# Kernel tuning notes

Measured on AMD Instinct MI355X. Metric: run time of the kernel, lower is better.

## Reference

```python
import jax, jax.numpy as jnp
import numpy as np

D_MODEL = 1024
NHEAD = 16
D_HEAD = D_MODEL // NHEAD


def setup_inputs() -> dict:
    key = jax.random.key(0)
    ks = jax.random.split(key, 9)
    B, S = 2, 2048
    scale = 1.0 / np.sqrt(D_MODEL)
    x = jax.random.normal(ks[0], (B, S, D_MODEL), dtype=jnp.float32)
    Wq = jax.random.normal(ks[1], (D_MODEL, D_MODEL), dtype=jnp.float32) * scale
    Wk = jax.random.normal(ks[2], (D_MODEL, D_MODEL), dtype=jnp.float32) * scale
    Wv = jax.random.normal(ks[3], (D_MODEL, D_MODEL), dtype=jnp.float32) * scale
    Wo = jax.random.normal(ks[4], (D_MODEL, D_MODEL), dtype=jnp.float32) * scale
    bq = jax.random.normal(ks[5], (D_MODEL,), dtype=jnp.float32) * 0.01
    bk = jax.random.normal(ks[6], (D_MODEL,), dtype=jnp.float32) * 0.01
    bv = jax.random.normal(ks[7], (D_MODEL,), dtype=jnp.float32) * 0.01
    bo = jax.random.normal(ks[8], (D_MODEL,), dtype=jnp.float32) * 0.01
    return {"x": x, "Wq": Wq, "bq": bq, "Wk": Wk, "bk": bk,
            "Wv": Wv, "bv": bv, "Wo": Wo, "bo": bo}


def reference(x, Wq, bq, Wk, bk, Wv, bv, Wo, bo):
    B, S, D = x.shape
    H, Dh = NHEAD, D_HEAD
    # projections; weights stored as (in, out) so y = x @ W + b
    def split_heads(t):  # [B,S,D] -> [B,H,S,Dh]
        return t.reshape(B, S, H, Dh).transpose(0, 2, 1, 3)
    q = split_heads(x @ Wq + bq)
    k = split_heads(x @ Wk + bk)
    v = split_heads(x @ Wv + bv)
    scale = 1.0 / jnp.sqrt(jnp.asarray(Dh, dtype=x.dtype))
    attn = jnp.einsum("bhqd,bhkd->bhqk", q, k) * scale  # [B,H,S,S]
    attn = jax.nn.softmax(attn, axis=-1)
    out = jnp.einsum("bhqk,bhkd->bhqd", attn, v)  # [B,H,S,Dh]
    out = out.transpose(0, 2, 1, 3).reshape(B, S, D)
    return out @ Wo + bo
```

## Files before the change

### kernel.cpp

```cpp
#include <hip/hip_runtime.h>
#include <hip/hip_bf16.h>
#include <stdint.h>
#include <stddef.h>

typedef __bf16 b16;
typedef __bf16 b16x4 __attribute__((ext_vector_type(4)));
typedef __bf16 b16x8 __attribute__((ext_vector_type(8)));
typedef short  s16x4 __attribute__((ext_vector_type(4)));
typedef float  f32x4 __attribute__((ext_vector_type(4)));

#define LOG2E 1.4426950408889634f
#define QSCALE (0.125f * LOG2E)

#if __has_builtin(__builtin_amdgcn_exp2f)
#define EXP2F(x) __builtin_amdgcn_exp2f(x)
#else
#define EXP2F(x) exp2f(x)
#endif

typedef __attribute__((address_space(1))) void gvoid;
typedef __attribute__((address_space(3))) void svoid;

__device__ __forceinline__ void async_cp16(void* lds, const void* g) {
    __builtin_amdgcn_global_load_lds((gvoid*)(void*)g, (svoid*)lds, 16, 0, 0);
}

__global__ __launch_bounds__(256) void k_cvt_x(const float* __restrict__ x,
                                               b16* __restrict__ xb) {
    int i = (blockIdx.x * 256 + threadIdx.x) * 4;
    float4 v = *(const float4*)(x + i);
    b16x4 o = { (b16)v.x, (b16)v.y, (b16)v.z, (b16)v.w };
    *(b16x4*)(xb + i) = o;
}

__global__ __launch_bounds__(256) void k_transpose(const float* __restrict__ Wq,
                                                   const float* __restrict__ Wk,
                                                   const float* __restrict__ Wv,
                                                   const float* __restrict__ Wo,
                                                   b16* __restrict__ WtQKV,
                                                   b16* __restrict__ Wot) {
    __shared__ float t[32][33];
    const int z = blockIdx.z;
    const float* W = (z == 0) ? Wq : (z == 1) ? Wk : (z == 2) ? Wv : Wo;
    const int k0 = blockIdx.x * 32, n0 = blockIdx.y * 32;
    const int tr = threadIdx.x >> 3, tc4 = (threadIdx.x & 7) * 4;
    float4 v = *(const float4*)(W + (size_t)(k0 + tr) * 1024 + n0 + tc4);
    t[tr][tc4 + 0] = v.x; t[tr][tc4 + 1] = v.y;
    t[tr][tc4 + 2] = v.z; t[tr][tc4 + 3] = v.w;
    __syncthreads();
    b16* dst = (z < 3) ? (WtQKV + ((size_t)z << 20)) : Wot;
    b16x4 o = { (b16)t[tc4 + 0][tr], (b16)t[tc4 + 1][tr],
                (b16)t[tc4 + 2][tr], (b16)t[tc4 + 3][tr] };
    *(b16x4*)(dst + (size_t)(n0 + tr) * 1024 + k0 + tc4) = o;
}

__device__ __forceinline__ void gemm_stage(const b16* __restrict__ Ab,
                                           const b16* __restrict__ Bb,
                                           b16* As, b16* Bs, int buf, int k0, int tid) {
    const int ci0 = tid, ci1 = tid + 256;
    b16* Ad = As + buf * 4096;
    b16* Bd = Bs + buf * 4096;
    async_cp16(Ad + ci0 * 8, Ab + (size_t)(ci0 >> 2) * 1024 + k0 + (ci0 & 3) * 8);
    async_cp16(Ad + ci1 * 8, Ab + (size_t)(ci1 >> 2) * 1024 + k0 + (ci1 & 3) * 8);
    async_cp16(Bd + ci0 * 8, Bb + (size_t)(ci0 >> 2) * 1024 + k0 + (ci0 & 3) * 8);
    async_cp16(Bd + ci1 * 8, Bb + (size_t)(ci1 >> 2) * 1024 + k0 + (ci1 & 3) * 8);
}

__device__ __forceinline__ void gemm128_core(const b16* __restrict__ Ab,
                                             const b16* __restrict__ Bb,
                                             b16* As, b16* Bs, int tid,
                                             f32x4 acc[4][4]) {
    const int lane = tid & 63, wave = tid >> 6;
    const int wm = wave & 1, wn = wave >> 1;
    const int quad = lane >> 4, lc = lane & 15;
    gemm_stage(Ab, Bb, As, Bs, 0, 0, tid);
    int cur = 0;
    for (int k0 = 0; k0 < 1024; k0 += 32) {
        __syncthreads();
        if (k0 + 32 < 1024)
            gemm_stage(Ab, Bb, As, Bs, cur ^ 1, k0 + 32, tid);
        const b16* Ac = As + cur * 4096;
        const b16* Bc = Bs + cur * 4096;
        b16x8 af[4], bfr[4];
#pragma unroll
        for (int mt = 0; mt < 4; ++mt)
            af[mt] = *(const b16x8*)(Ac + (wm * 64 + mt * 16 + lc) * 32 + quad * 8);
#pragma unroll
        for (int nt = 0; nt < 4; ++nt)
            bfr[nt] = *(const b16x8*)(Bc + (wn * 64 + nt * 16 + lc) * 32 + quad * 8);
#pragma unroll
        for (int mt = 0; mt < 4; ++mt)
#pragma unroll
            for (int nt = 0; nt < 4; ++nt)
                acc[mt][nt] = __builtin_amdgcn_mfma_f32_16x16x32_bf16(
                    af[mt], bfr[nt], acc[mt][nt], 0, 0, 0);
        cur ^= 1;
    }
}

__global__ __launch_bounds__(256, 3) void k_gemm_qkv(
    const b16* __restrict__ A, const b16* __restrict__ Bt,
    const float* __restrict__ bq, const float* __restrict__ bk,
    const float* __restrict__ bv,
    b16* __restrict__ Qg, b16* __restrict__ Kg, b16* __restrict__ Vtg) {
    __shared__ __align__(16) b16 SM[2 * 128 * 32 * 2];
    b16* As = SM;
    b16* Bs = SM + 8192;
    const int bm = blockIdx.x, bn = blockIdx.y;
    const int tid = threadIdx.x;
    const int lane = tid & 63, wave = tid >> 6;
    const int wm = wave & 1, wn = wave >> 1;
    const int quad = lane >> 4, lc = lane & 15;

    f32x4 acc[4][4] = {};
    gemm128_core(A + (size_t)(bm * 128) * 1024, Bt + (size_t)(bn * 128) * 1024,
                 As, Bs, tid, acc);

    const int mat = bn >> 3;
    if (mat == 2) {
        b16* Sl = SM;
        const int b = (bm * 128) >> 11;
        const int s0 = (bm * 128) & 2047;
        const int bh2base = b * 16 + (bn - 16) * 2;
#pragma unroll
        for (int rd = 0; rd < 2; ++rd) {
            __syncthreads();
            if (wn == rd) {
#pragma unroll
                for (int nt = 0; nt < 4; ++nt) {
                    const int cm = (bn * 128 + wn * 64 + nt * 16 + lc) & 1023;
                    const float bval = bv[cm];
#pragma unroll
                    for (int mt = 0; mt < 4; ++mt) {
                        b16x4 o = { (b16)(acc[mt][nt][0] + bval),
                                    (b16)(acc[mt][nt][1] + bval),
                                    (b16)(acc[mt][nt][2] + bval),
                                    (b16)(acc[mt][nt][3] + bval) };
                        *(b16x4*)(Sl + (nt * 16 + lc) * 136 + wm * 64 + mt * 16 + quad * 4) = o;
                    }
                }
            }
            __syncthreads();
            const int bh2 = bh2base + rd;
#pragma unroll
            for (int p = 0; p < 4; ++p) {
                const int n = p * 16 + (tid >> 4), c = tid & 15;
                b16x8 v = *(const b16x8*)(Sl + n * 136 + c * 8);
                *(b16x8*)(Vtg + (size_t)(bh2 * 64 + n) * 2048 + s0 + c * 8) = v;
            }
        }
        return;
    }

    const float* bp = (mat == 0) ? bq : bk;
#pragma unroll
    for (int nt = 0; nt < 4; ++nt) {
        const int n = bn * 128 + wn * 64 + nt * 16 + lc;
        const int cm = n & 1023;
        const int h = cm >> 6, dh = cm & 63;
        const float bval = bp[cm];
#pragma unroll
        for (int mt = 0; mt < 4; ++mt) {
            const int m0 = bm * 128 + wm * 64 + mt * 16 + quad * 4;
            const int b = m0 >> 11;
            const int bh = b * 16 + h;
            const int s0 = m0 & 2047;
            if (mat == 0) {
#pragma unroll
                for (int r = 0; r < 4; ++r)
                    Qg[(size_t)(bh * 2048 + s0 + r) * 64 + dh] =
                        (b16)((acc[mt][nt][r] + bval) * QSCALE);
            } else {
#pragma unroll
                for (int r = 0; r < 4; ++r)
                    Kg[(size_t)(bh * 2048 + s0 + r) * 64 + dh] =
                        (b16)(acc[mt][nt][r] + bval);
            }
        }
    }
}

__global__ __launch_bounds__(256) void k_flash(
    const b16* __restrict__ Qg, const b16* __restrict__ Kg,
    const b16* __restrict__ Vtg, b16* __restrict__ AO) {
    __shared__ __align__(16) b16 Ks[2][64 * 64];
    __shared__ __align__(16) b16 Vs[2][64 * 64];
    __shared__ __align__(16) b16 Es[256 * 72];
    const int bh = blockIdx.x;
    const int qb = blockIdx.y;
    const int tid = threadIdx.x, lane = tid & 63, wave = tid >> 6;
    const int quad = lane >> 4, lc = lane & 15;

    const b16* Qbase = Qg + ((size_t)bh * 2048 + qb * 256 + wave * 64) * 64;
    b16x8 qf[4][2];
#pragma unroll
    for (int qt = 0; qt < 4; ++qt)
#pragma unroll
        for (int ch = 0; ch < 2; ++ch)
            qf[qt][ch] = *(const b16x8*)(Qbase + (qt * 16 + lc) * 64 + ch * 32 + quad * 8);

    f32x4 oacc[4][4] = {};
    float lsum[4] = {0.f, 0.f, 0.f, 0.f};

    const b16* Kbh = Kg + (size_t)bh * 2048 * 64;
    const b16* Vbh = Vtg + (size_t)bh * 64 * 2048;

    const int ciA = tid, ciB = tid + 256;
    const int rA = ciA >> 3, gA = (ciA & 7) ^ (rA & 7);
    const int rB = ciB >> 3, gB = (ciB & 7) ^ (rB & 7);

    async_cp16(&Ks[0][ciA * 8], Kbh + (size_t)(rA) * 64 + gA * 8);
    async_cp16(&Ks[0][ciB * 8], Kbh + (size_t)(rB) * 64 + gB * 8);
    async_cp16(&Vs[0][ciA * 8], Vbh + (size_t)rA * 2048 + gA * 8);
    async_cp16(&Vs[0][ciB * 8], Vbh + (size_t)rB * 2048 + gB * 8);
    int cur = 0;

    for (int kt = 0; kt < 32; ++kt) {
        __syncthreads();
        if (kt + 1 < 32) {
            const int nk = kt + 1, nb = cur ^ 1;
            async_cp16(&Ks[nb][ciA * 8], Kbh + (size_t)(nk * 64 + rA) * 64 + gA * 8);
            async_cp16(&Ks[nb][ciB * 8], Kbh + (size_t)(nk * 64 + rB) * 64 + gB * 8);
            async_cp16(&Vs[nb][ciA * 8], Vbh + (size_t)rA * 2048 + nk * 64 + gA * 8);
            async_cp16(&Vs[nb][ciB * 8], Vbh + (size_t)rB * 2048 + nk * 64 + gB * 8);
        }

        const b16* Kc = Ks[cur];
        const b16* Vc = Vs[cur];
#pragma unroll
        for (int m = 0; m < 4; ++m) {
            const int row = m * 16 + lc;
            const b16x8 kf0 = *(const b16x8*)(Kc + row * 64 + ((quad) ^ (row & 7)) * 8);
            const b16x8 kf1 = *(const b16x8*)(Kc + row * 64 + ((4 + quad) ^ (row & 7)) * 8);

            s16x4 pb[4];
#pragma unroll
            for (int qt = 0; qt < 4; ++qt) {
                f32x4 s = {};
                s = __builtin_amdgcn_mfma_f32_16x16x32_bf16(kf0, qf[qt][0], s, 0, 0, 0);
                s = __builtin_amdgcn_mfma_f32_16x16x32_bf16(kf1, qf[qt][1], s, 0, 0, 0);
                const float e0 = EXP2F(s[0]), e1 = EXP2F(s[1]);
                const float e2 = EXP2F(s[2]), e3 = EXP2F(s[3]);
                lsum[qt] += (e0 + e1) + (e2 + e3);
                b16x4 p = { (b16)e0, (b16)e1, (b16)e2, (b16)e3 };
                pb[qt] = __builtin_bit_cast(s16x4, p);
            }
            s16x4 vf[4];
#pragma unroll
            for (int dt = 0; dt < 4; ++dt) {
                const int vrow = dt * 16 + lc;
                const int chunk = (m * 2 + (quad >> 1)) ^ (vrow & 7);
                vf[dt] = *(const s16x4*)(Vc + vrow * 64 + chunk * 8 + (quad & 1) * 4);
            }
#pragma unroll
            for (int dt = 0; dt < 4; ++dt)
#pragma unroll
                for (int qt = 0; qt < 4; ++qt)
                    oacc[dt][qt] = __builtin_amdgcn_mfma_f32_16x16x16bf16_1k(
                        vf[dt], pb[qt], oacc[dt][qt], 0, 0, 0);
        }
        cur ^= 1;
    }

#pragma unroll
    for (int qt = 0; qt < 4; ++qt) {
        lsum[qt] += __shfl_xor(lsum[qt], 16, 64);
        lsum[qt] += __shfl_xor(lsum[qt], 32, 64);
    }

    const int b = bh >> 4, h = bh & 15;
#pragma unroll
    for (int qt = 0; qt < 4; ++qt) {
        const float inv = 1.0f / lsum[qt];
        const int qrow = wave * 64 + qt * 16 + lc;
#pragma unroll
        for (int dt = 0; dt < 4; ++dt) {
            b16x4 ob = { (b16)(oacc[dt][qt][0] * inv), (b16)(oacc[dt][qt][1] * inv),
                         (b16)(oacc[dt][qt][2] * inv), (b16)(oacc[dt][qt][3] * inv) };
            *(b16x4*)(Es + qrow * 72 + dt * 16 + quad * 4) = ob;
        }
    }
    __syncthreads();
    const size_t aobase = (size_t)(b * 2048 + qb * 256) * 1024 + h * 64;
#pragma unroll
    for (int p = 0; p < 8; ++p) {
        const int q = p * 32 + (tid >> 3);
        const int c = tid & 7;
        b16x8 v = *(const b16x8*)(Es + q * 72 + c * 8);
        *(b16x8*)(AO + aobase + (size_t)q * 1024 + c * 8) = v;
    }
}

__global__ __launch_bounds__(256, 2) void k_gemm_out(
    const b16* __restrict__ A, const b16* __restrict__ Bt,
    const float* __restrict__ bo, float* __restrict__ out) {
    __shared__ __align__(16) b16 As[2 * 64 * 32];
    __shared__ __align__(16) b16 Bs[2 * 128 * 32];
    const int bm = blockIdx.x, bn = blockIdx.y;
    const int tid = threadIdx.x;
    const int lane = tid & 63, wave = tid >> 6;
    const int wm = wave & 1, wn = wave >> 1;
    const int quad = lane >> 4, lc = lane & 15;
    const b16* Ab = A + (size_t)(bm * 64) * 1024;
    const b16* Bb = Bt + (size_t)(bn * 128) * 1024;

    const int ci0 = tid, ci1 = tid + 256;
    async_cp16(&As[ci0 * 8], Ab + (size_t)(ci0 >> 2) * 1024 + (ci0 & 3) * 8);
    async_cp16(&Bs[ci0 * 8], Bb + (size_t)(ci0 >> 2) * 1024 + (ci0 & 3) * 8);
    async_cp16(&Bs[ci1 * 8], Bb + (size_t)(ci1 >> 2) * 1024 + (ci1 & 3) * 8);

    f32x4 acc[2][4] = {};
    int cur = 0;
    for (int k0 = 0; k0 < 1024; k0 += 32) {
        __syncthreads();
        if (k0 + 32 < 1024) {
            const int kn = k0 + 32, nb = cur ^ 1;
            async_cp16(&As[nb * 2048 + ci0 * 8], Ab + (size_t)(ci0 >> 2) * 1024 + kn + (ci0 & 3) * 8);
            async_cp16(&Bs[nb * 4096 + ci0 * 8], Bb + (size_t)(ci0 >> 2) * 1024 + kn + (ci0 & 3) * 8);
            async_cp16(&Bs[nb * 4096 + ci1 * 8], Bb + (size_t)(ci1 >> 2) * 1024 + kn + (ci1 & 3) * 8);
        }
        const b16* Ac = &As[cur * 2048];
        const b16* Bc = &Bs[cur * 4096];
        b16x8 af[2], bfr[4];
#pragma unroll
        for (int mt = 0; mt < 2; ++mt)
            af[mt] = *(const b16x8*)(Ac + (wm * 32 + mt * 16 + lc) * 32 + quad * 8);
#pragma unroll
        for (int nt = 0; nt < 4; ++nt)
            bfr[nt] = *(const b16x8*)(Bc + (wn * 64 + nt * 16 + lc) * 32 + quad * 8);
#pragma unroll
        for (int mt = 0; mt < 2; ++mt)
#pragma unroll
            for (int nt = 0; nt < 4; ++nt)
                acc[mt][nt] = __builtin_amdgcn_mfma_f32_16x16x32_bf16(
                    af[mt], bfr[nt], acc[mt][nt], 0, 0, 0);
        cur ^= 1;
    }

#pragma unroll
    for (int nt = 0; nt < 4; ++nt) {
        const int n = bn * 128 + wn * 64 + nt * 16 + lc;
        const float bval = bo[n];
#pragma unroll
        for (int mt = 0; mt < 2; ++mt) {
            const int m0 = bm * 64 + wm * 32 + mt * 16 + quad * 4;
#pragma unroll
            for (int r = 0; r < 4; ++r)
                out[(size_t)(m0 + r) * 1024 + n] = acc[mt][nt][r] + bval;
        }
    }
}

extern "C" void kernel_launch(void* const* d_in, const int* in_sizes, int n_in,
                              void* d_out, int out_size, void* d_ws, size_t ws_size,
                              hipStream_t stream) {
    const float* x  = (const float*)d_in[0];
    const float* Wq = (const float*)d_in[1];
    const float* bq = (const float*)d_in[2];
    const float* Wk = (const float*)d_in[3];
    const float* bk = (const float*)d_in[4];
    const float* Wv = (const float*)d_in[5];
    const float* bv = (const float*)d_in[6];
    const float* Wo = (const float*)d_in[7];
    const float* bo = (const float*)d_in[8];
    float* out = (float*)d_out;

    char* ws = (char*)d_ws;
    const size_t MB = 1024 * 1024;
    b16* Xb  = (b16*)(ws);
    b16* AO  = (b16*)(ws);
    b16* WtQ = (b16*)(ws + 8 * MB);
    b16* Wot = (b16*)(ws + 14 * MB);
    b16* Qg  = (b16*)(ws + 16 * MB);
    b16* Kg  = (b16*)(ws + 24 * MB);
    b16* Vtg = (b16*)(ws + 32 * MB);

    k_cvt_x<<<4096, 256, 0, stream>>>(x, Xb);
    k_transpose<<<dim3(32, 32, 4), 256, 0, stream>>>(Wq, Wk, Wv, Wo, WtQ, Wot);
    k_gemm_qkv<<<dim3(32, 24), 256, 0, stream>>>(Xb, WtQ, bq, bk, bv, Qg, Kg, Vtg);
    k_flash<<<dim3(32, 8), 256, 0, stream>>>(Qg, Kg, Vtg, AO);
    k_gemm_out<<<dim3(64, 8), 256, 0, stream>>>(AO, Wot, bo, out);
}
```

Before: 208.7 us.

## Use 8 waves per flash block, compute row sums via MFMA, swap GEMM grid order

The flash kernel now runs 512 threads per block, with each wave owning 32 query rows instead of 64. This halves per-wave accumulator registers and doubles the waves per block that share the same K/V tiles. The softmax denominator is now accumulated with an extra MFMA against a vector of ones, replacing the per-element float adds and cross-lane shuffles. The QKV and output GEMM grids swap block-index order so that consecutive blocks share the same activation rows, which may improve L2 reuse. The ones-MFMA sums the bf16-rounded probabilities rather than the fp32 values, a small numerical change.

```diff
diff --git a/kernel.cpp b/kernel.cpp
--- a/kernel.cpp
+++ b/kernel.cpp
@@ -106,7 +106,7 @@
     __shared__ __align__(16) b16 SM[2 * 128 * 32 * 2];
     b16* As = SM;
     b16* Bs = SM + 8192;
-    const int bm = blockIdx.x, bn = blockIdx.y;
+    const int bn = blockIdx.x, bm = blockIdx.y;
     const int tid = threadIdx.x;
     const int lane = tid & 63, wave = tid >> 6;
     const int wm = wave & 1, wn = wave >> 1;
@@ -180,7 +180,7 @@
     }
 }
 
-__global__ __launch_bounds__(256) void k_flash(
+__global__ __launch_bounds__(512) void k_flash(
     const b16* __restrict__ Qg, const b16* __restrict__ Kg,
     const b16* __restrict__ Vtg, b16* __restrict__ AO) {
     __shared__ __align__(16) b16 Ks[2][64 * 64];
@@ -191,38 +191,35 @@
     const int tid = threadIdx.x, lane = tid & 63, wave = tid >> 6;
     const int quad = lane >> 4, lc = lane & 15;
 
-    const b16* Qbase = Qg + ((size_t)bh * 2048 + qb * 256 + wave * 64) * 64;
-    b16x8 qf[4][2];
-#pragma unroll
-    for (int qt = 0; qt < 4; ++qt)
+    const b16* Qbase = Qg + ((size_t)bh * 2048 + qb * 256 + wave * 32) * 64;
+    b16x8 qf[2][2];
+#pragma unroll
+    for (int qt = 0; qt < 2; ++qt)
 #pragma unroll
         for (int ch = 0; ch < 2; ++ch)
             qf[qt][ch] = *(const b16x8*)(Qbase + (qt * 16 + lc) * 64 + ch * 32 + quad * 8);
 
-    f32x4 oacc[4][4] = {};
-    float lsum[4] = {0.f, 0.f, 0.f, 0.f};
+    f32x4 oacc[4][2] = {};
+    f32x4 lacc[2] = {};
+    const s16x4 ones = { (short)0x3F80, (short)0x3F80,
+                         (short)0x3F80, (short)0x3F80 };
 
     const b16* Kbh = Kg + (size_t)bh * 2048 * 64;
     const b16* Vbh = Vtg + (size_t)bh * 64 * 2048;
 
-    const int ciA = tid, ciB = tid + 256;
-    const int rA = ciA >> 3, gA = (ciA & 7) ^ (rA & 7);
-    const int rB = ciB >> 3, gB = (ciB & 7) ^ (rB & 7);
-
-    async_cp16(&Ks[0][ciA * 8], Kbh + (size_t)(rA) * 64 + gA * 8);
-    async_cp16(&Ks[0][ciB * 8], Kbh + (size_t)(rB) * 64 + gB * 8);
-    async_cp16(&Vs[0][ciA * 8], Vbh + (size_t)rA * 2048 + gA * 8);
-    async_cp16(&Vs[0][ciB * 8], Vbh + (size_t)rB * 2048 + gB * 8);
+    const int ci = tid;
+    const int rS = ci >> 3, gS = (ci & 7) ^ (rS & 7);
+
+    async_cp16(&Ks[0][ci * 8], Kbh + (size_t)rS * 64 + gS * 8);
+    async_cp16(&Vs[0][ci * 8], Vbh + (size_t)rS * 2048 + gS * 8);
     int cur = 0;
 
     for (int kt = 0; kt < 32; ++kt) {
         __syncthreads();
         if (kt + 1 < 32) {
             const int nk = kt + 1, nb = cur ^ 1;
-            async_cp16(&Ks[nb][ciA * 8], Kbh + (size_t)(nk * 64 + rA) * 64 + gA * 8);
-            async_cp16(&Ks[nb][ciB * 8], Kbh + (size_t)(nk * 64 + rB) * 64 + gB * 8);
-            async_cp16(&Vs[nb][ciA * 8], Vbh + (size_t)rA * 2048 + nk * 64 + gA * 8);
-            async_cp16(&Vs[nb][ciB * 8], Vbh + (size_t)rB * 2048 + nk * 64 + gB * 8);
+            async_cp16(&Ks[nb][ci * 8], Kbh + (size_t)(nk * 64 + rS) * 64 + gS * 8);
+            async_cp16(&Vs[nb][ci * 8], Vbh + (size_t)rS * 2048 + nk * 64 + gS * 8);
         }
 
         const b16* Kc = Ks[cur];
@@ -233,16 +230,14 @@
             const b16x8 kf0 = *(const b16x8*)(Kc + row * 64 + ((quad) ^ (row & 7)) * 8);
             const b16x8 kf1 = *(const b16x8*)(Kc + row * 64 + ((4 + quad) ^ (row & 7)) * 8);
 
-            s16x4 pb[4];
-#pragma unroll
-            for (int qt = 0; qt < 4; ++qt) {
+            s16x4 pb[2];
+#pragma unroll
+            for (int qt = 0; qt < 2; ++qt) {
                 f32x4 s = {};
                 s = __builtin_amdgcn_mfma_f32_16x16x32_bf16(kf0, qf[qt][0], s, 0, 0, 0);
                 s = __builtin_amdgcn_mfma_f32_16x16x32_bf16(kf1, qf[qt][1], s, 0, 0, 0);
-                const float e0 = EXP2F(s[0]), e1 = EXP2F(s[1]);
-                const float e2 = EXP2F(s[2]), e3 = EXP2F(s[3]);
-                lsum[qt] += (e0 + e1) + (e2 + e3);
-                b16x4 p = { (b16)e0, (b16)e1, (b16)e2, (b16)e3 };
+                b16x4 p = { (b16)EXP2F(s[0]), (b16)EXP2F(s[1]),
+                            (b16)EXP2F(s[2]), (b16)EXP2F(s[3]) };
                 pb[qt] = __builtin_bit_cast(s16x4, p);
             }
             s16x4 vf[4];
@@ -255,24 +250,22 @@
 #pragma unroll
             for (int dt = 0; dt < 4; ++dt)
 #pragma unroll
-                for (int qt = 0; qt < 4; ++qt)
+                for (int qt = 0; qt < 2; ++qt)
                     oacc[dt][qt] = __builtin_amdgcn_mfma_f32_16x16x16bf16_1k(
                         vf[dt], pb[qt], oacc[dt][qt], 0, 0, 0);
+#pragma unroll
+            for (int qt = 0; qt < 2; ++qt)
+                lacc[qt] = __builtin_amdgcn_mfma_f32_16x16x16bf16_1k(
+                    ones, pb[qt], lacc[qt], 0, 0, 0);
         }
         cur ^= 1;
     }
 
-#pragma unroll
-    for (int qt = 0; qt < 4; ++qt) {
-        lsum[qt] += __shfl_xor(lsum[qt], 16, 64);
-        lsum[qt] += __shfl_xor(lsum[qt], 32, 64);
-    }
-
     const int b = bh >> 4, h = bh & 15;
 #pragma unroll
-    for (int qt = 0; qt < 4; ++qt) {
-        const float inv = 1.0f / lsum[qt];
-        const int qrow = wave * 64 + qt * 16 + lc;
+    for (int qt = 0; qt < 2; ++qt) {
+        const float inv = 1.0f / lacc[qt][0];
+        const int qrow = wave * 32 + qt * 16 + lc;
 #pragma unroll
         for (int dt = 0; dt < 4; ++dt) {
             b16x4 ob = { (b16)(oacc[dt][qt][0] * inv), (b16)(oacc[dt][qt][1] * inv),
@@ -283,8 +276,8 @@
     __syncthreads();
     const size_t aobase = (size_t)(b * 2048 + qb * 256) * 1024 + h * 64;
 #pragma unroll
-    for (int p = 0; p < 8; ++p) {
-        const int q = p * 32 + (tid >> 3);
+    for (int p = 0; p < 4; ++p) {
+        const int q = p * 64 + (tid >> 3);
         const int c = tid & 7;
         b16x8 v = *(const b16x8*)(Es + q * 72 + c * 8);
         *(b16x8*)(AO + aobase + (size_t)q * 1024 + c * 8) = v;
@@ -296,7 +289,7 @@
     const float* __restrict__ bo, float* __restrict__ out) {
     __shared__ __align__(16) b16 As[2 * 64 * 32];
     __shared__ __align__(16) b16 Bs[2 * 128 * 32];
-    const int bm = blockIdx.x, bn = blockIdx.y;
+    const int bn = blockIdx.x, bm = blockIdx.y;
     const int tid = threadIdx.x;
     const int lane = tid & 63, wave = tid >> 6;
     const int wm = wave & 1, wn = wave >> 1;
@@ -377,7 +370,7 @@
 
     k_cvt_x<<<4096, 256, 0, stream>>>(x, Xb);
     k_transpose<<<dim3(32, 32, 4), 256, 0, stream>>>(Wq, Wk, Wv, Wo, WtQ, Wot);
-    k_gemm_qkv<<<dim3(32, 24), 256, 0, stream>>>(Xb, WtQ, bq, bk, bv, Qg, Kg, Vtg);
-    k_flash<<<dim3(32, 8), 256, 0, stream>>>(Qg, Kg, Vtg, AO);
-    k_gemm_out<<<dim3(64, 8), 256, 0, stream>>>(AO, Wot, bo, out);
-}
+    k_gemm_qkv<<<dim3(24, 32), 256, 0, stream>>>(Xb, WtQ, bq, bk, bv, Qg, Kg, Vtg);
+    k_flash<<<dim3(32, 8), 512, 0, stream>>>(Qg, Kg, Vtg, AO);
+    k_gemm_out<<<dim3(8, 64), 256, 0, stream>>>(AO, Wot, bo, out);
+}
```

Result: no change. 204.7 us (-1.9%).
